# Optimization experiments

Measured on AMD Instinct MI355X. Metric: run time of the kernel, lower is better.

## Reference

```python
import jax, jax.numpy as jnp
import numpy as np

N_NODES = 100000
N_EDGES = 1600000
DIM_IN = 128
DIM_OUT = 128


def setup_inputs() -> dict:
    key = jax.random.key(0)
    k_x, k_e, k_w = jax.random.split(key, 3)
    x = jax.random.normal(k_x, (N_NODES, DIM_IN), dtype=jnp.float32)
    edge_index = jax.random.randint(k_e, (2, N_EDGES), 0, N_NODES, dtype=jnp.int64)
    # Glorot-uniform weight like PyG's GCNConv linear layer, stored [d_in, d_out]
    limit = np.sqrt(6.0 / (DIM_IN + DIM_OUT)).astype(np.float32)
    W = jax.random.uniform(k_w, (DIM_IN, DIM_OUT), dtype=jnp.float32, minval=-limit, maxval=limit)
    return {"x": x, "edge_index": edge_index, "W": W}


def reference(x, edge_index, W):
    # PyG GCNConv (bias=False): out = D^{-1/2} (A + I) D^{-1/2} (x @ W)
    N = x.shape[0]
    x_proj = x @ W  # [N, d_out]
    loop = jnp.arange(N, dtype=edge_index.dtype)
    src = jnp.concatenate([edge_index[0], loop])  # message sources (row)
    dst = jnp.concatenate([edge_index[1], loop])  # aggregation targets (col)
    # degree counted at target nodes (edge weight = 1), incl. self loops
    deg = jax.ops.segment_sum(jnp.ones(src.shape, dtype=x.dtype), dst, num_segments=N)
    dis = jnp.where(deg > 0, jax.lax.rsqrt(deg), 0.0)
    norm = dis[src] * dis[dst]  # [E+N]
    msgs = x_proj[src] * norm[:, None]  # [E+N, d_out] gather + scale
    return jax.ops.segment_sum(msgs, dst, num_segments=N)  # scatter-add
```

## Files before the change

kernel.cpp:

```cpp
#include <hip/hip_runtime.h>
#include <hip/hip_bf16.h>

#define DIM 128
#define PCH 4096

typedef __attribute__((ext_vector_type(8))) short bf16x8;
typedef __attribute__((ext_vector_type(4))) float f32x4;

__device__ __forceinline__ float bfu_lo(unsigned u) { return __uint_as_float(u << 16); }
__device__ __forceinline__ float bfu_hi(unsigned u) { return __uint_as_float(u & 0xffff0000u); }
__device__ __forceinline__ unsigned short f2bf(float f) {
    unsigned u = __float_as_uint(f);
    u += 0x7fffu + ((u >> 16) & 1u);
    return (unsigned short)(u >> 16);
}

__device__ __forceinline__ int edge_at(const void* ei, int idx64, long long pos) {
    return idx64 ? (int)__builtin_nontemporal_load((const long long*)ei + pos)
                 : __builtin_nontemporal_load((const int*)ei + pos);
}

__device__ __forceinline__ int detect_idx64(const void* ei, int E, unsigned* s_or, int* s_flag) {
    const unsigned* ei_w = (const unsigned*)ei;
    int t = threadIdx.x;
    unsigned o = 0;
    int lim = (E < 4096) ? E : 4096;
    for (int k = t; k < lim; k += 256) o |= ei_w[2 * k + 1];
    s_or[t] = o;
    __syncthreads();
    for (int s = 128; s > 0; s >>= 1) {
        if (t < s) s_or[t] |= s_or[t + s];
        __syncthreads();
    }
    if (t == 0) *s_flag = (s_or[0] == 0u) ? 1 : 0;
    __syncthreads();
    return *s_flag;
}

__global__ __launch_bounds__(256) void hist_detect(const void* ei, unsigned* bcnt,
                                                   int E, int shift) {
    __shared__ unsigned s_h[512];
    __shared__ unsigned s_or[256];
    __shared__ int s_flag;
    int t = threadIdx.x;
    for (int i = t; i < 512; i += 256) s_h[i] = 0u;
    int idx64 = detect_idx64(ei, E, s_or, &s_flag);
    long long stride = (long long)gridDim.x * 256;
    for (long long e = (long long)blockIdx.x * 256 + t; e < E; e += stride) {
        int d = edge_at(ei, idx64, (long long)E + e);
        atomicAdd(&s_h[d >> shift], 1u);
    }
    __syncthreads();
    for (int i = t; i < 512; i += 256)
        if (s_h[i]) atomicAdd(&bcnt[i], s_h[i]);
}

__global__ __launch_bounds__(256) void partition(const void* ei, const unsigned* __restrict__ bcnt,
                                                 unsigned* bcur0, long long* pout,
                                                 int E, int B, int shift) {
    __shared__ unsigned s_hist[512], s_off[512], s_gbase[512], s_pref[512], s_bbase[512];
    __shared__ unsigned wsum[4];
    __shared__ unsigned s_or[256];
    __shared__ int s_flag;
    __shared__ long long s_p[PCH];
    int t = threadIdx.x;
    long long base = (long long)blockIdx.x * PCH;
    for (int i = t; i < 512; i += 256) { s_hist[i] = 0u; s_off[i] = 0u; }
    int idx64 = detect_idx64(ei, E, s_or, &s_flag);

    {
        unsigned v0 = bcnt[2 * t], v1 = bcnt[2 * t + 1];
        unsigned ps = v0 + v1;
        unsigned s = ps;
        int lane = t & 63;
#pragma unroll
        for (int off = 1; off < 64; off <<= 1) {
            unsigned u = __shfl_up(s, off, 64);
            if (lane >= off) s += u;
        }
        int w = t >> 6;
        if (lane == 63) wsum[w] = s;
        __syncthreads();
        unsigned woff = 0;
        for (int j = 0; j < w; j++) woff += wsum[j];
        unsigned excl = woff + s - ps;
        s_bbase[2 * t] = excl;
        s_bbase[2 * t + 1] = excl + v0;
    }
    __syncthreads();

    int d_[PCH / 256], s_[PCH / 256];
#pragma unroll 4
    for (int j = 0; j < PCH / 256; j++) {
        long long e = base + j * 256 + t;
        if (e < E) {
            d_[j] = edge_at(ei, idx64, (long long)E + e);
            s_[j] = edge_at(ei, idx64, e);
            atomicAdd(&s_hist[d_[j] >> shift], 1u);
        } else d_[j] = -1;
    }
    __syncthreads();

    {
        unsigned v0 = s_hist[2 * t], v1 = s_hist[2 * t + 1];
        unsigned ps = v0 + v1;
        unsigned s = ps;
        int lane = t & 63;
#pragma unroll
        for (int off = 1; off < 64; off <<= 1) {
            unsigned u = __shfl_up(s, off, 64);
            if (lane >= off) s += u;
        }
        int w = t >> 6;
        if (lane == 63) wsum[w] = s;
        __syncthreads();
        unsigned woff = 0;
        for (int j = 0; j < w; j++) woff += wsum[j];
        unsigned excl = woff + s - ps;
        s_pref[2 * t] = excl;
        s_pref[2 * t + 1] = excl + v0;
    }
    __syncthreads();

    for (int i = t; i < B; i += 256)
        if (s_hist[i]) s_gbase[i] = s_bbase[i] + atomicAdd(&bcur0[i], s_hist[i]);
#pragma unroll 4
    for (int j = 0; j < PCH / 256; j++)
        if (d_[j] >= 0) {
            int b = d_[j] >> shift;
            unsigned p = s_pref[b] + atomicAdd(&s_off[b], 1u);
            s_p[p] = ((long long)s_[j] << 32) | (unsigned)d_[j];
        }
    __syncthreads();
    long long rem = (long long)E - base;
    unsigned tot = (rem < PCH) ? (unsigned)rem : (unsigned)PCH;
    for (unsigned i = t; i < tot; i += 256) {
        int lo = 0, hi = B - 1;
        while (lo < hi) {
            int mid = (lo + hi + 1) >> 1;
            if (s_pref[mid] <= i) lo = mid; else hi = mid - 1;
        }
        pout[s_gbase[lo] + (i - s_pref[lo])] = s_p[i];
    }
}

__global__ __launch_bounds__(256) void build_csr(const long long* __restrict__ pairs,
                                                 const unsigned* __restrict__ bcnt,
                                                 unsigned* deg, unsigned* row_start,
                                                 float* dis, int* col_src,
                                                 int N, int shift) {
    __shared__ unsigned cnt[512], cur[512], pref[512];
    __shared__ unsigned s_bb[513];
    __shared__ unsigned wsum[4];
    int b = blockIdx.x, t = threadIdx.x;
    int npb = 1 << shift;
    if (npb > 512) npb = 512;
    int nodeLo = b << shift;

    {
        unsigned v0 = bcnt[2 * t], v1 = bcnt[2 * t + 1];
        unsigned ps = v0 + v1;
        unsigned s = ps;
        int lane = t & 63;
#pragma unroll
        for (int off = 1; off < 64; off <<= 1) {
            unsigned u = __shfl_up(s, off, 64);
            if (lane >= off) s += u;
        }
        int w = t >> 6;
        if (lane == 63) wsum[w] = s;
        __syncthreads();
        unsigned woff = 0;
        for (int j = 0; j < w; j++) woff += wsum[j];
        unsigned excl = woff + s - ps;
        s_bb[2 * t] = excl;
        s_bb[2 * t + 1] = excl + v0;
        if (t == 255) s_bb[512] = excl + ps;
    }
    __syncthreads();
    unsigned lo = s_bb[b], hi = s_bb[b + 1];

    for (int i = t; i < npb; i += 256) cnt[i] = 0u;
    __syncthreads();
    for (unsigned e = lo + t; e < hi; e += 256) {
        int d = (int)pairs[e];
        atomicAdd(&cnt[d - nodeLo], 1u);
    }
    __syncthreads();
    unsigned v0 = (2 * t < npb) ? cnt[2 * t] : 0u;
    unsigned v1 = (2 * t + 1 < npb) ? cnt[2 * t + 1] : 0u;
    unsigned ps = v0 + v1;
    unsigned s = ps;
    int lane = t & 63;
#pragma unroll
    for (int off = 1; off < 64; off <<= 1) {
        unsigned u = __shfl_up(s, off, 64);
        if (lane >= off) s += u;
    }
    int w = t >> 6;
    if (lane == 63) wsum[w] = s;
    __syncthreads();
    unsigned woff = 0;
    for (int j = 0; j < w; j++) woff += wsum[j];
    unsigned excl = woff + s - ps;
    if (2 * t < npb) pref[2 * t] = excl;
    if (2 * t + 1 < npb) pref[2 * t + 1] = excl + v0;
    __syncthreads();
    for (int i = t; i < npb; i += 256) {
        int node = nodeLo + i;
        unsigned rs = lo + pref[i];
        if (node < N) {
            unsigned c = cnt[i];
            deg[node] = c;
            row_start[node] = rs;
            dis[node] = rsqrtf((float)c + 1.0f);
        }
        cur[i] = rs;
    }
    __syncthreads();
    for (unsigned e = lo + t; e < hi; e += 256) {
        long long v = pairs[e];
        int d = (int)v;
        int sv = (int)(v >> 32);
        unsigned pos = atomicAdd(&cur[d - nodeLo], 1u);
        col_src[pos] = sv;
    }
}

__global__ __launch_bounds__(256) void gemm_xw(const float* __restrict__ x,
                                               const float* __restrict__ W,
                                               const float* __restrict__ dis,
                                               unsigned short* __restrict__ xps, int N) {
    __shared__ unsigned short wt[128 * 136];
    int tid = threadIdx.x;
    for (int idx = tid; idx < DIM * DIM; idx += 256) {
        int k = idx >> 7, n = idx & 127;
        wt[n * 136 + k] = f2bf(W[idx]);
    }
    __syncthreads();

    int wv = tid >> 6, lane = tid & 63;
    int l15 = lane & 15, quad = lane >> 4;
    int rowBase = blockIdx.x * 128 + wv * 32;

    f32x4 acc[2][8];
#pragma unroll
    for (int mt = 0; mt < 2; mt++)
#pragma unroll
        for (int nt = 0; nt < 8; nt++)
            acc[mt][nt] = (f32x4){0.f, 0.f, 0.f, 0.f};

#pragma unroll
    for (int k0 = 0; k0 < DIM; k0 += 32) {
        bf16x8 aa[2], bb[8];
#pragma unroll
        for (int mt = 0; mt < 2; mt++) {
            int r = rowBase + mt * 16 + l15;
            if (r > N - 1) r = N - 1;
            const float* xf = x + (size_t)r * DIM + k0 + quad * 8;
            float4 u0 = ((const float4*)xf)[0];
            float4 u1 = ((const float4*)xf)[1];
            bf16x8 a;
            a[0] = (short)f2bf(u0.x); a[1] = (short)f2bf(u0.y);
            a[2] = (short)f2bf(u0.z); a[3] = (short)f2bf(u0.w);
            a[4] = (short)f2bf(u1.x); a[5] = (short)f2bf(u1.y);
            a[6] = (short)f2bf(u1.z); a[7] = (short)f2bf(u1.w);
            aa[mt] = a;
        }
#pragma unroll
        for (int nt = 0; nt < 8; nt++)
            bb[nt] = *(const bf16x8*)(wt + (nt * 16 + l15) * 136 + k0 + quad * 8);
#pragma unroll
        for (int mt = 0; mt < 2; mt++)
#pragma unroll
            for (int nt = 0; nt < 8; nt++)
                acc[mt][nt] = __builtin_amdgcn_mfma_f32_16x16x32_bf16(bb[nt], aa[mt], acc[mt][nt], 0, 0, 0);
    }

#pragma unroll
    for (int mt = 0; mt < 2; mt++) {
        int r = rowBase + mt * 16 + l15;
        if (r < N) {
            float sc = dis[r];
#pragma unroll
            for (int nt = 0; nt < 8; nt++) {
                int c0 = nt * 16 + quad * 4;
                ushort4 o;
                o.x = f2bf(acc[mt][nt][0] * sc);
                o.y = f2bf(acc[mt][nt][1] * sc);
                o.z = f2bf(acc[mt][nt][2] * sc);
                o.w = f2bf(acc[mt][nt][3] * sc);
                *(ushort4*)(xps + (size_t)r * DIM + c0) = o;
            }
        }
    }
}

__global__ __launch_bounds__(256) void aggregate(const unsigned short* __restrict__ xps,
                                                 const unsigned* __restrict__ row_start,
                                                 const unsigned* __restrict__ deg,
                                                 const float* __restrict__ dis,
                                                 const int* __restrict__ col_src,
                                                 float* __restrict__ out, int N) {
    int wid = (int)((blockIdx.x * 256 + threadIdx.x) >> 6);
    if (wid >= N) return;
    int lane = threadIdx.x & 63;
    int grp = lane >> 4, lin = lane & 15;
    const uint4* xp4 = (const uint4*)xps;

    float acc[8];
#pragma unroll
    for (int j = 0; j < 8; j++) acc[j] = 0.f;

    unsigned rs = row_start[wid];
    unsigned cnt = deg[wid];
    unsigned tot = cnt + 1;

    for (unsigned base = 0; base < tot; base += 64) {
        unsigned slot = base + (unsigned)lane;
        int idx = (slot < cnt) ? col_src[rs + slot] : wid;
        unsigned rem = tot - base; if (rem > 64) rem = 64;
        unsigned kmax = (rem + 7) >> 3;

        uint4 v0[8], v1[8];
        float m0[8], m1[8];
#pragma unroll
        for (int q = 0; q < 8; q++) {
            if ((unsigned)q < kmax) {
                unsigned sl0 = q * 8 + (unsigned)grp;
                unsigned sl1 = sl0 + 4;
                int s0 = __shfl(idx, (int)sl0, 64);
                int s1 = __shfl(idx, (int)sl1, 64);
                m0[q] = (sl0 < rem) ? 1.f : 0.f;
                m1[q] = (sl1 < rem) ? 1.f : 0.f;
                v0[q] = xp4[(size_t)s0 * 16 + lin];
                v1[q] = xp4[(size_t)s1 * 16 + lin];
            }
        }
#pragma unroll
        for (int q = 0; q < 8; q++) {
            if ((unsigned)q < kmax) {
                acc[0] = fmaf(bfu_lo(v0[q].x), m0[q], acc[0]);
                acc[1] = fmaf(bfu_hi(v0[q].x), m0[q], acc[1]);
                acc[2] = fmaf(bfu_lo(v0[q].y), m0[q], acc[2]);
                acc[3] = fmaf(bfu_hi(v0[q].y), m0[q], acc[3]);
                acc[4] = fmaf(bfu_lo(v0[q].z), m0[q], acc[4]);
                acc[5] = fmaf(bfu_hi(v0[q].z), m0[q], acc[5]);
                acc[6] = fmaf(bfu_lo(v0[q].w), m0[q], acc[6]);
                acc[7] = fmaf(bfu_hi(v0[q].w), m0[q], acc[7]);
                acc[0] = fmaf(bfu_lo(v1[q].x), m1[q], acc[0]);
                acc[1] = fmaf(bfu_hi(v1[q].x), m1[q], acc[1]);
                acc[2] = fmaf(bfu_lo(v1[q].y), m1[q], acc[2]);
                acc[3] = fmaf(bfu_hi(v1[q].y), m1[q], acc[3]);
                acc[4] = fmaf(bfu_lo(v1[q].z), m1[q], acc[4]);
                acc[5] = fmaf(bfu_hi(v1[q].z), m1[q], acc[5]);
                acc[6] = fmaf(bfu_lo(v1[q].w), m1[q], acc[6]);
                acc[7] = fmaf(bfu_hi(v1[q].w), m1[q], acc[7]);
            }
        }
    }

#pragma unroll
    for (int j = 0; j < 8; j++) {
        acc[j] += __shfl_xor(acc[j], 16, 64);
        acc[j] += __shfl_xor(acc[j], 32, 64);
    }

    float di = dis[wid];
    if (grp < 2) {
        int jb = (grp & 1) * 4;
        float4 o;
        o.x = acc[jb + 0] * di;
        o.y = acc[jb + 1] * di;
        o.z = acc[jb + 2] * di;
        o.w = acc[jb + 3] * di;
        *(float4*)(out + (size_t)wid * DIM + lin * 8 + jb) = o;
    }
}

extern "C" void kernel_launch(void* const* d_in, const int* in_sizes, int n_in,
                              void* d_out, int out_size, void* d_ws, size_t ws_size,
                              hipStream_t stream) {
    const int N = in_sizes[0] / DIM;
    const int E = in_sizes[1] / 2;
    const float* x = (const float*)d_in[0];
    const void* ei = d_in[1];
    const float* W = (const float*)d_in[2];
    float* out = (float*)d_out;

    int shift = 8;
    while ((((long long)N + (1LL << shift) - 1) >> shift) > 512 && shift < 9) shift++;
    int B = (int)(((long long)N + (1LL << shift) - 1) >> shift);

    char* wsp = (char*)d_ws;
    size_t off = 0;
    auto alloc = [&](size_t b) { void* p = wsp + off; off += (b + 255) & ~(size_t)255; return p; };
    unsigned* bcnt       = (unsigned*)alloc(4096);
    unsigned* bcur0      = bcnt + 512;
    unsigned* deg        = (unsigned*)alloc((size_t)N * 4);
    unsigned* row_start  = (unsigned*)alloc((size_t)N * 4);
    float*    dis        = (float*)alloc((size_t)N * 4);
    int*      col_src    = (int*)alloc((size_t)E * 4);
    unsigned short* xps  = (unsigned short*)alloc((size_t)N * DIM * 2);

    long long* pairs = (long long*)xps;
    if ((size_t)E * 8 > (size_t)N * DIM * 2 && off + (size_t)E * 8 <= ws_size)
        pairs = (long long*)alloc((size_t)E * 8);

    hipMemsetAsync(bcnt, 0, 4096, stream);
    hist_detect<<<512, 256, 0, stream>>>(ei, bcnt, E, shift);
    partition<<<(E + PCH - 1) / PCH, 256, 0, stream>>>(ei, bcnt, bcur0, pairs, E, B, shift);
    build_csr<<<B, 256, 0, stream>>>(pairs, bcnt, deg, row_start, dis, col_src, N, shift);
    gemm_xw<<<(N + 127) / 128, 256, 0, stream>>>(x, W, dis, xps, N);
    aggregate<<<(N + 3) / 4, 256, 0, stream>>>(xps, row_start, deg, dis, col_src, out, N);
}
```

Baseline: 297.7 us.

## Enlarge CSR buckets, drop bucket binary search, software-pipeline neighbor gather

Partition scatter now computes each pair's bucket directly from its destination instead of binary-searching the prefix array. Bucket size grows to 2048 nodes, with fixed-size shared arrays and a per-thread 8-element scan in the CSR build. The aggregation loop switches from loading eight neighbor rows at once to a one-ahead prefetch, which cuts register pressure but reduces the number of outstanding loads. Fewer, larger buckets lower build_csr parallelism.

```diff
diff --git a/kernel.cpp b/kernel.cpp
--- a/kernel.cpp
+++ b/kernel.cpp
@@ -3,6 +3,7 @@
 
 #define DIM 128
 #define PCH 4096
+#define NPB 2048
 
 typedef __attribute__((ext_vector_type(8))) short bf16x8;
 typedef __attribute__((ext_vector_type(4))) float f32x4;
@@ -135,12 +136,9 @@
     long long rem = (long long)E - base;
     unsigned tot = (rem < PCH) ? (unsigned)rem : (unsigned)PCH;
     for (unsigned i = t; i < tot; i += 256) {
-        int lo = 0, hi = B - 1;
-        while (lo < hi) {
-            int mid = (lo + hi + 1) >> 1;
-            if (s_pref[mid] <= i) lo = mid; else hi = mid - 1;
-        }
-        pout[s_gbase[lo] + (i - s_pref[lo])] = s_p[i];
+        long long v = s_p[i];
+        int b = ((int)v) >> shift;
+        pout[s_gbase[b] + (i - s_pref[b])] = v;
     }
 }
 
@@ -149,12 +147,10 @@
                                                  unsigned* deg, unsigned* row_start,
                                                  float* dis, int* col_src,
                                                  int N, int shift) {
-    __shared__ unsigned cnt[512], cur[512], pref[512];
+    __shared__ unsigned cnt[NPB], cur[NPB], pref[NPB];
     __shared__ unsigned s_bb[513];
     __shared__ unsigned wsum[4];
     int b = blockIdx.x, t = threadIdx.x;
-    int npb = 1 << shift;
-    if (npb > 512) npb = 512;
     int nodeLo = b << shift;
 
     {
@@ -180,33 +176,41 @@
     __syncthreads();
     unsigned lo = s_bb[b], hi = s_bb[b + 1];
 
-    for (int i = t; i < npb; i += 256) cnt[i] = 0u;
+#pragma unroll
+    for (int j = 0; j < NPB / 256; j++) cnt[t + j * 256] = 0u;
     __syncthreads();
     for (unsigned e = lo + t; e < hi; e += 256) {
         int d = (int)pairs[e];
         atomicAdd(&cnt[d - nodeLo], 1u);
     }
     __syncthreads();
-    unsigned v0 = (2 * t < npb) ? cnt[2 * t] : 0u;
-    unsigned v1 = (2 * t + 1 < npb) ? cnt[2 * t + 1] : 0u;
-    unsigned ps = v0 + v1;
-    unsigned s = ps;
-    int lane = t & 63;
-#pragma unroll
-    for (int off = 1; off < 64; off <<= 1) {
-        unsigned u = __shfl_up(s, off, 64);
-        if (lane >= off) s += u;
-    }
-    int w = t >> 6;
-    if (lane == 63) wsum[w] = s;
-    __syncthreads();
-    unsigned woff = 0;
-    for (int j = 0; j < w; j++) woff += wsum[j];
-    unsigned excl = woff + s - ps;
-    if (2 * t < npb) pref[2 * t] = excl;
-    if (2 * t + 1 < npb) pref[2 * t + 1] = excl + v0;
-    __syncthreads();
-    for (int i = t; i < npb; i += 256) {
+
+    {
+        unsigned loc[8];
+        unsigned run = 0;
+#pragma unroll
+        for (int j = 0; j < 8; j++) { loc[j] = run; run += cnt[t * 8 + j]; }
+        unsigned s = run;
+        int lane = t & 63;
+#pragma unroll
+        for (int off = 1; off < 64; off <<= 1) {
+            unsigned u = __shfl_up(s, off, 64);
+            if (lane >= off) s += u;
+        }
+        int w = t >> 6;
+        if (lane == 63) wsum[w] = s;
+        __syncthreads();
+        unsigned woff = 0;
+        for (int j = 0; j < w; j++) woff += wsum[j];
+        unsigned tbase = woff + s - run;
+#pragma unroll
+        for (int j = 0; j < 8; j++) pref[t * 8 + j] = tbase + loc[j];
+    }
+    __syncthreads();
+
+#pragma unroll
+    for (int j = 0; j < NPB / 256; j++) {
+        int i = t + j * 256;
         int node = nodeLo + i;
         unsigned rs = lo + pref[i];
         if (node < N) {
@@ -322,40 +326,46 @@
         unsigned rem = tot - base; if (rem > 64) rem = 64;
         unsigned kmax = (rem + 7) >> 3;
 
-        uint4 v0[8], v1[8];
-        float m0[8], m1[8];
+        int p0 = __shfl(idx, grp, 64);
+        int p1 = __shfl(idx, grp + 4, 64);
+        float ma0 = ((unsigned)grp < rem) ? 1.f : 0.f;
+        float ma1 = ((unsigned)(grp + 4) < rem) ? 1.f : 0.f;
+        uint4 a0 = xp4[(size_t)p0 * 16 + lin];
+        uint4 a1 = xp4[(size_t)p1 * 16 + lin];
+
 #pragma unroll
         for (int q = 0; q < 8; q++) {
             if ((unsigned)q < kmax) {
-                unsigned sl0 = q * 8 + (unsigned)grp;
-                unsigned sl1 = sl0 + 4;
-                int s0 = __shfl(idx, (int)sl0, 64);
-                int s1 = __shfl(idx, (int)sl1, 64);
-                m0[q] = (sl0 < rem) ? 1.f : 0.f;
-                m1[q] = (sl1 < rem) ? 1.f : 0.f;
-                v0[q] = xp4[(size_t)s0 * 16 + lin];
-                v1[q] = xp4[(size_t)s1 * 16 + lin];
-            }
-        }
-#pragma unroll
-        for (int q = 0; q < 8; q++) {
-            if ((unsigned)q < kmax) {
-                acc[0] = fmaf(bfu_lo(v0[q].x), m0[q], acc[0]);
-                acc[1] = fmaf(bfu_hi(v0[q].x), m0[q], acc[1]);
-                acc[2] = fmaf(bfu_lo(v0[q].y), m0[q], acc[2]);
-                acc[3] = fmaf(bfu_hi(v0[q].y), m0[q], acc[3]);
-                acc[4] = fmaf(bfu_lo(v0[q].z), m0[q], acc[4]);
-                acc[5] = fmaf(bfu_hi(v0[q].z), m0[q], acc[5]);
-                acc[6] = fmaf(bfu_lo(v0[q].w), m0[q], acc[6]);
-                acc[7] = fmaf(bfu_hi(v0[q].w), m0[q], acc[7]);
-                acc[0] = fmaf(bfu_lo(v1[q].x), m1[q], acc[0]);
-                acc[1] = fmaf(bfu_hi(v1[q].x), m1[q], acc[1]);
-                acc[2] = fmaf(bfu_lo(v1[q].y), m1[q], acc[2]);
-                acc[3] = fmaf(bfu_hi(v1[q].y), m1[q], acc[3]);
-                acc[4] = fmaf(bfu_lo(v1[q].z), m1[q], acc[4]);
-                acc[5] = fmaf(bfu_hi(v1[q].z), m1[q], acc[5]);
-                acc[6] = fmaf(bfu_lo(v1[q].w), m1[q], acc[6]);
-                acc[7] = fmaf(bfu_hi(v1[q].w), m1[q], acc[7]);
+                uint4 b0, b1;
+                float mb0 = 0.f, mb1 = 0.f;
+                bool pf = ((unsigned)(q + 1) < kmax);
+                if (pf) {
+                    unsigned sl0 = (unsigned)(q + 1) * 8 + (unsigned)grp;
+                    unsigned sl1 = sl0 + 4;
+                    int t0 = __shfl(idx, (int)sl0, 64);
+                    int t1 = __shfl(idx, (int)sl1, 64);
+                    mb0 = (sl0 < rem) ? 1.f : 0.f;
+                    mb1 = (sl1 < rem) ? 1.f : 0.f;
+                    b0 = xp4[(size_t)t0 * 16 + lin];
+                    b1 = xp4[(size_t)t1 * 16 + lin];
+                }
+                acc[0] = fmaf(bfu_lo(a0.x), ma0, acc[0]);
+                acc[1] = fmaf(bfu_hi(a0.x), ma0, acc[1]);
+                acc[2] = fmaf(bfu_lo(a0.y), ma0, acc[2]);
+                acc[3] = fmaf(bfu_hi(a0.y), ma0, acc[3]);
+                acc[4] = fmaf(bfu_lo(a0.z), ma0, acc[4]);
+                acc[5] = fmaf(bfu_hi(a0.z), ma0, acc[5]);
+                acc[6] = fmaf(bfu_lo(a0.w), ma0, acc[6]);
+                acc[7] = fmaf(bfu_hi(a0.w), ma0, acc[7]);
+                acc[0] = fmaf(bfu_lo(a1.x), ma1, acc[0]);
+                acc[1] = fmaf(bfu_hi(a1.x), ma1, acc[1]);
+                acc[2] = fmaf(bfu_lo(a1.y), ma1, acc[2]);
+                acc[3] = fmaf(bfu_hi(a1.y), ma1, acc[3]);
+                acc[4] = fmaf(bfu_lo(a1.z), ma1, acc[4]);
+                acc[5] = fmaf(bfu_hi(a1.z), ma1, acc[5]);
+                acc[6] = fmaf(bfu_lo(a1.w), ma1, acc[6]);
+                acc[7] = fmaf(bfu_hi(a1.w), ma1, acc[7]);
+                if (pf) { a0 = b0; a1 = b1; ma0 = mb0; ma1 = mb1; }
             }
         }
     }
@@ -388,8 +398,8 @@
     const float* W = (const float*)d_in[2];
     float* out = (float*)d_out;
 
-    int shift = 8;
-    while ((((long long)N + (1LL << shift) - 1) >> shift) > 512 && shift < 9) shift++;
+    int shift = 11;
+    while ((((long long)N + (1LL << shift) - 1) >> shift) > 512) shift++;
     int B = (int)(((long long)N + (1LL << shift) - 1) >> shift);
 
     char* wsp = (char*)d_ws;
```

Measured after the change: 312.7 us. 5.0% more time.
